# Optimization experiments

Hardware: AMD Instinct MI355X
Metric: run time of the kernel (lower is better)

Reference implementation:

```python
import jax, jax.numpy as jnp
import numpy as np

N, IN_DIM, HID, OUT_DIM, E, L = 100000, 128, 128, 64, 1600000, 4
ALPHA = 0.6


def gcn_conv(x, W, b, src, dst, deg_inv_sqrt):
    # PyG GCNConv: add self-loops, symmetric norm, linear, scatter-add, bias
    xw = x @ W                                    # [N, H]
    norm = deg_inv_sqrt[src] * deg_inv_sqrt[dst]  # [E]
    msg = xw[src] * norm[:, None]                 # [E, H] (memory-bound gather)
    agg = jax.ops.segment_sum(msg, dst, num_segments=N)
    # self-loop contribution: weight 1 * deg^-1
    agg = agg + xw * (deg_inv_sqrt * deg_inv_sqrt)[:, None]
    return agg + b


def setup_inputs() -> dict:
    key = jax.random.key(0)
    ks = jax.random.split(key, 8)
    s = 1.0 / np.sqrt(HID)
    x = jax.random.normal(ks[0], (N, IN_DIM), dtype=jnp.float32)
    edge_index = jax.random.randint(ks[1], (2, E), 0, N, dtype=jnp.int64)
    W1 = jax.random.uniform(ks[2], (IN_DIM, HID), jnp.float32, -s, s)
    b1 = jnp.zeros((HID,), jnp.float32)
    convW = jax.random.uniform(ks[3], (L, HID, HID), jnp.float32, -s, s)
    convB = jnp.zeros((L, HID), jnp.float32)
    W2 = jax.random.uniform(ks[4], (HID, OUT_DIM), jnp.float32, -s, s)
    b2 = jnp.zeros((OUT_DIM,), jnp.float32)
    return {"x": x, "edge_index": edge_index, "W1": W1, "b1": b1,
            "convW": convW, "convB": convB, "W2": W2, "b2": b2}


def reference(x, edge_index, W1, b1, convW, convB, W2, b2):
    src, dst = edge_index[0], edge_index[1]
    # degree with self-loops (gcn_norm with edge weight 1 on dst/col)
    deg = jax.ops.segment_sum(jnp.ones((E,), x.dtype), dst, num_segments=N) + 1.0
    deg_inv_sqrt = 1.0 / jnp.sqrt(deg)

    Z = x @ W1 + b1
    z_init = Z
    z_sum = jnp.zeros_like(Z)
    for i in range(L):
        Z = jax.nn.relu(gcn_conv(Z, convW[i], convB[i], src, dst, deg_inv_sqrt))
        z_sum = z_sum + Z
    out = ALPHA * z_init + (1.0 - ALPHA) * z_sum / L
    return out @ W2 + b2
```

## Files before the change

### kernel.cpp

```cpp
#include <hip/hip_runtime.h>

#define HID 128
#define NLAYERS 4
#define MAXBUCK 1600
#define CHUNK 16384

typedef __attribute__((ext_vector_type(8))) short bf16x8;
typedef __attribute__((ext_vector_type(8))) unsigned short u16x8;
typedef __attribute__((ext_vector_type(4))) float f32x4;

static __device__ __forceinline__ float bf2f(unsigned short u) {
    return __uint_as_float(((unsigned)u) << 16);
}
static __device__ __forceinline__ unsigned short f2bf(float f) {
    unsigned u = __float_as_uint(f);
    return (unsigned short)((u + 0x7FFF + ((u >> 16) & 1)) >> 16);
}


__global__ __launch_bounds__(256) void bin1(const int* __restrict__ dst,
                                            int* __restrict__ cnt2d, int E, int nbuck) {
    __shared__ int h[MAXBUCK];
    int tid = threadIdx.x;
    for (int i = tid; i < nbuck; i += 256) h[i] = 0;
    __syncthreads();
    int e0 = blockIdx.x * CHUNK;
    int e1 = min(e0 + CHUNK, E);
    for (int e = e0 + tid; e < e1; e += 256) atomicAdd(&h[dst[e] >> 6], 1);
    __syncthreads();
    for (int i = tid; i < nbuck; i += 256)
        cnt2d[(size_t)blockIdx.x * nbuck + i] = h[i];
}

__global__ void colscan(int* __restrict__ cnt2d, int* __restrict__ colsum,
                        int nchunks, int nbuck) {
    int b = blockIdx.x * blockDim.x + threadIdx.x;
    if (b >= nbuck) return;
    int run = 0;
    for (int c = 0; c < nchunks; ++c) {
        size_t idx = (size_t)c * nbuck + b;
        int v = cnt2d[idx];
        cnt2d[idx] = run;
        run += v;
    }
    colsum[b] = run;
}

__global__ __launch_bounds__(256) void basescan(const int* __restrict__ colsum,
                                                int* __restrict__ base, int nbuck) {
    __shared__ int part[256];
    int tid = threadIdx.x;
    const int per = 7;
    int loc[per];
    int run = 0;
    for (int i = 0; i < per; ++i) {
        int idx = tid * per + i;
        int v = (idx < nbuck) ? colsum[idx] : 0;
        run += v;
        loc[i] = run;
    }
    part[tid] = run;
    __syncthreads();
    for (int off = 1; off < 256; off <<= 1) {
        int t = (tid >= off) ? part[tid - off] : 0;
        __syncthreads();
        part[tid] += t;
        __syncthreads();
    }
    int prev = tid ? part[tid - 1] : 0;
    if (tid == 0) base[0] = 0;
    for (int i = 0; i < per; ++i) {
        int idx = tid * per + i;
        if (idx < nbuck) base[idx + 1] = prev + loc[i];
    }
}

__global__ __launch_bounds__(256) void bin2(const int* __restrict__ src, const int* __restrict__ dst,
                                            const int* __restrict__ cnt2d, const int* __restrict__ base,
                                            unsigned* __restrict__ ecoarse, int E, int nbuck) {
    __shared__ int cur[MAXBUCK];
    int tid = threadIdx.x;
    for (int i = tid; i < nbuck; i += 256)
        cur[i] = base[i] + cnt2d[(size_t)blockIdx.x * nbuck + i];
    __syncthreads();
    int e0 = blockIdx.x * CHUNK;
    int e1 = min(e0 + CHUNK, E);
    for (int e = e0 + tid; e < e1; e += 256) {
        int d = dst[e];
        int b = d >> 6;
        int pos = atomicAdd(&cur[b], 1);
        ecoarse[pos] = (unsigned)src[e] | ((unsigned)(d & 63) << 20);
    }
}

__global__ __launch_bounds__(64) void degdis(const unsigned* __restrict__ ecoarse,
                                             const int* __restrict__ base,
                                             float* __restrict__ dis, int N) {
    __shared__ int cnt[64];
    int b = blockIdx.x, t = threadIdx.x;
    cnt[t] = 0;
    __syncthreads();
    int s = base[b], e = base[b + 1];
    for (int i = s + t; i < e; i += 64) atomicAdd(&cnt[ecoarse[i] >> 20], 1);
    __syncthreads();
    int node = b * 64 + t;
    if (node < N) dis[node] = rsqrtf((float)cnt[t] + 1.0f);
}

__global__ __launch_bounds__(256) void finesort(const unsigned* __restrict__ ecoarse,
                                                const int* __restrict__ base,
                                                const float* __restrict__ dis,
                                                int2* __restrict__ csr, int* __restrict__ rowp,
                                                int N, int E) {
    __shared__ int h[64], off[64];
    int b = blockIdx.x, tid = threadIdx.x;
    if (tid < 64) h[tid] = 0;
    __syncthreads();
    int s = base[b], e = base[b + 1];
    for (int i = s + tid; i < e; i += 256) atomicAdd(&h[ecoarse[i] >> 20], 1);
    __syncthreads();
    if (tid == 0) {
        int run = 0;
        for (int i = 0; i < 64; ++i) { off[i] = run; run += h[i]; }
    }
    __syncthreads();
    int node = b * 64 + tid;
    if (tid < 64 && node < N) rowp[node] = s + off[tid];
    if (b == 0 && tid == 0) rowp[N] = E;
    if (tid < 64) h[tid] = off[tid];
    __syncthreads();
    for (int i = s + tid; i < e; i += 256) {
        unsigned v = ecoarse[i];
        int srcn = v & 0xFFFFF;
        int dl = v >> 20;
        int pos = atomicAdd(&h[dl], 1);
        int2 o;
        o.x = srcn;
        o.y = __float_as_int(dis[srcn] * dis[b * 64 + dl]);
        csr[s + pos] = o;
    }
}


__global__ void wprep(const float* __restrict__ W1, const float* __restrict__ convW,
                      const float* __restrict__ W2, unsigned short* __restrict__ W1t,
                      unsigned short* __restrict__ convWt, unsigned short* __restrict__ W2t) {
    int r = blockIdx.x;
    int k = threadIdx.x;
    const float* src;
    unsigned short* dst;
    int ncols, n;
    if (r < 128) { src = W1; dst = W1t; n = r; ncols = 128; }
    else if (r < 640) {
        int l = (r - 128) >> 7; n = (r - 128) & 127;
        src = convW + (size_t)l * 16384; dst = convWt + (size_t)l * 16384; ncols = 128;
    } else { src = W2; dst = W2t; n = r - 640; ncols = 64; }
    dst[(size_t)n * 128 + k] = f2bf(src[(size_t)k * ncols + n]);
}

__global__ void xcast(const float* __restrict__ x, unsigned short* __restrict__ xb, int n8) {
    int i = blockIdx.x * blockDim.x + threadIdx.x;
    if (i >= n8) return;
    float4 v0 = *(const float4*)&x[(size_t)i * 8];
    float4 v1 = *(const float4*)&x[(size_t)i * 8 + 4];
    u16x8 o;
    o[0] = f2bf(v0.x); o[1] = f2bf(v0.y); o[2] = f2bf(v0.z); o[3] = f2bf(v0.w);
    o[4] = f2bf(v1.x); o[5] = f2bf(v1.y); o[6] = f2bf(v1.z); o[7] = f2bf(v1.w);
    *(u16x8*)&xb[(size_t)i * 8] = o;
}


template <bool BIAS>
__global__ __launch_bounds__(256, 2) void gemm128_mfma(
    const unsigned short* __restrict__ A, const unsigned short* __restrict__ Bt,
    const float* __restrict__ bias, unsigned short* __restrict__ C, int nrows) {
    int wid = threadIdx.x >> 6, lane = threadIdx.x & 63;
    int l15 = lane & 15, l4 = lane >> 4;

    bf16x8 b[8][4];
#pragma unroll
    for (int nt = 0; nt < 8; ++nt)
#pragma unroll
        for (int ks = 0; ks < 4; ++ks)
            b[nt][ks] = *(const bf16x8*)&Bt[(size_t)(nt * 16 + l15) * 128 + ks * 32 + l4 * 8];
    float bb[8];
    if (BIAS) {
#pragma unroll
        for (int nt = 0; nt < 8; ++nt) bb[nt] = bias[nt * 16 + l15];
    }

    for (int s2 = 0; s2 < 2; ++s2) {
        int row0 = (blockIdx.x * 8 + wid * 2 + s2) * 16;
        if (row0 >= nrows) break;
        int ar = min(row0 + l15, nrows - 1);
        bf16x8 a[4];
#pragma unroll
        for (int ks = 0; ks < 4; ++ks)
            a[ks] = *(const bf16x8*)&A[(size_t)ar * 128 + ks * 32 + l4 * 8];
        f32x4 acc[8] = {};
#pragma unroll
        for (int ks = 0; ks < 4; ++ks)
#pragma unroll
            for (int nt = 0; nt < 8; ++nt)
                acc[nt] = __builtin_amdgcn_mfma_f32_16x16x32_bf16(a[ks], b[nt][ks], acc[nt], 0, 0, 0);
#pragma unroll
        for (int nt = 0; nt < 8; ++nt) {
            int col = nt * 16 + l15;
#pragma unroll
            for (int r = 0; r < 4; ++r) {
                int row = row0 + l4 * 4 + r;
                if (row < nrows) {
                    float v = acc[nt][r];
                    if (BIAS) v += bb[nt];
                    C[(size_t)row * 128 + col] = f2bf(v);
                }
            }
        }
    }
}


__global__ __launch_bounds__(256, 2) void gemm_final(
    const unsigned short* __restrict__ z0, const unsigned short* __restrict__ z1,
    const unsigned short* __restrict__ z2, const unsigned short* __restrict__ z3,
    const unsigned short* __restrict__ z4, const unsigned short* __restrict__ Bt,
    const float* __restrict__ bias, float* __restrict__ out, int nrows) {
    int wid = threadIdx.x >> 6, lane = threadIdx.x & 63;
    int l15 = lane & 15, l4 = lane >> 4;

    bf16x8 b[4][4];
#pragma unroll
    for (int nt = 0; nt < 4; ++nt)
#pragma unroll
        for (int ks = 0; ks < 4; ++ks)
            b[nt][ks] = *(const bf16x8*)&Bt[(size_t)(nt * 16 + l15) * 128 + ks * 32 + l4 * 8];
    float bb[4];
#pragma unroll
    for (int nt = 0; nt < 4; ++nt) bb[nt] = bias[nt * 16 + l15];

    const unsigned short* zs[5] = { z0, z1, z2, z3, z4 };

    for (int s2 = 0; s2 < 2; ++s2) {
        int row0 = (blockIdx.x * 8 + wid * 2 + s2) * 16;
        if (row0 >= nrows) break;
        int ar = min(row0 + l15, nrows - 1);
        bf16x8 a[5][4];
#pragma unroll
        for (int st = 0; st < 5; ++st)
#pragma unroll
            for (int ks = 0; ks < 4; ++ks)
                a[st][ks] = *(const bf16x8*)&zs[st][(size_t)ar * 128 + ks * 32 + l4 * 8];
        f32x4 acc0[4] = {};
        f32x4 acc1[4] = {};
#pragma unroll
        for (int st = 0; st < 5; ++st)
#pragma unroll
            for (int ks = 0; ks < 4; ++ks)
#pragma unroll
                for (int nt = 0; nt < 4; ++nt) {
                    if (st == 0)
                        acc0[nt] = __builtin_amdgcn_mfma_f32_16x16x32_bf16(a[0][ks], b[nt][ks], acc0[nt], 0, 0, 0);
                    else
                        acc1[nt] = __builtin_amdgcn_mfma_f32_16x16x32_bf16(a[st][ks], b[nt][ks], acc1[nt], 0, 0, 0);
                }
#pragma unroll
        for (int nt = 0; nt < 4; ++nt) {
            int col = nt * 16 + l15;
#pragma unroll
            for (int r = 0; r < 4; ++r) {
                int row = row0 + l4 * 4 + r;
                if (row < nrows)
                    out[(size_t)row * 64 + col] = 0.6f * acc0[nt][r] + 0.1f * acc1[nt][r] + bb[nt];
            }
        }
    }
}


__global__ __launch_bounds__(256) void spmm_kernel(
    const unsigned short* __restrict__ xwb, const int* __restrict__ rowp,
    const int2* __restrict__ csr, const float* __restrict__ dis,
    const float* __restrict__ bias, unsigned short* __restrict__ Z, int n) {
    int l = threadIdx.x & 15;
    int node = blockIdx.x * 16 + (threadIdx.x >> 4);
    if (node >= n) return;
    const u16x8* xw8 = (const u16x8*)xwb;

    float acc[8] = {};
    int beg = rowp[node], end = rowp[node + 1];
    int e = beg;
    for (; e + 4 <= end; e += 4) {
        int2 s0 = csr[e];
        int2 s1 = csr[e + 1];
        int2 s2 = csr[e + 2];
        int2 s3 = csr[e + 3];
        u16x8 x0 = xw8[(size_t)s0.x * 16 + l];
        u16x8 x1 = xw8[(size_t)s1.x * 16 + l];
        u16x8 x2 = xw8[(size_t)s2.x * 16 + l];
        u16x8 x3 = xw8[(size_t)s3.x * 16 + l];
        float w0 = __int_as_float(s0.y);
        float w1 = __int_as_float(s1.y);
        float w2 = __int_as_float(s2.y);
        float w3 = __int_as_float(s3.y);
#pragma unroll
        for (int j = 0; j < 8; ++j) {
            acc[j] = fmaf(w0, bf2f(x0[j]), acc[j]);
            acc[j] = fmaf(w1, bf2f(x1[j]), acc[j]);
            acc[j] = fmaf(w2, bf2f(x2[j]), acc[j]);
            acc[j] = fmaf(w3, bf2f(x3[j]), acc[j]);
        }
    }
    for (; e < end; ++e) {
        int2 s0 = csr[e];
        u16x8 x0 = xw8[(size_t)s0.x * 16 + l];
        float w0 = __int_as_float(s0.y);
#pragma unroll
        for (int j = 0; j < 8; ++j) acc[j] = fmaf(w0, bf2f(x0[j]), acc[j]);
    }

    float d = dis[node];
    float d2 = d * d;
    u16x8 xs = xw8[(size_t)node * 16 + l];
    float4 b0 = *(const float4*)&bias[l * 8];
    float4 b1 = *(const float4*)&bias[l * 8 + 4];
    float bbv[8] = { b0.x, b0.y, b0.z, b0.w, b1.x, b1.y, b1.z, b1.w };
    u16x8 ov;
#pragma unroll
    for (int j = 0; j < 8; ++j)
        ov[j] = f2bf(fmaxf(acc[j] + fmaf(d2, bf2f(xs[j]), bbv[j]), 0.f));
    *(u16x8*)&Z[(size_t)node * HID + l * 8] = ov;
}


extern "C" void kernel_launch(void* const* d_in, const int* in_sizes, int n_in,
                              void* d_out, int out_size, void* d_ws, size_t ws_size,
                              hipStream_t stream) {
    const float* x     = (const float*)d_in[0];
    const int*   ei    = (const int*)d_in[1];
    const float* W1    = (const float*)d_in[2];
    const float* b1    = (const float*)d_in[3];
    const float* convW = (const float*)d_in[4];
    const float* convB = (const float*)d_in[5];
    const float* W2    = (const float*)d_in[6];
    const float* b2    = (const float*)d_in[7];

    const int N = in_sizes[0] / HID;
    const int E = in_sizes[1] / 2;
    const int* src = ei;
    const int* dst = ei + E;
    const int nbuck = (N + 63) / 64;
    const int nchunks = (E + CHUNK - 1) / CHUNK;

    char* p = (char*)d_ws;
    auto alloc = [&](size_t bytes) {
        void* q = (void*)p;
        p += (bytes + 255) & ~(size_t)255;
        return q;
    };
    float* dis      = (float*)alloc((size_t)N * 4);
    int*   rowp     = (int*)alloc((size_t)(N + 1) * 4);
    int*   base     = (int*)alloc((size_t)(nbuck + 1) * 4);
    int*   colsum   = (int*)alloc((size_t)nbuck * 4);
    int*   cnt2d    = (int*)alloc((size_t)nchunks * nbuck * 4);
    unsigned* ecoarse = (unsigned*)alloc((size_t)E * 4);
    int2*  csr      = (int2*)alloc((size_t)E * 8);
    unsigned short* xb = (unsigned short*)alloc((size_t)N * HID * 2);
    unsigned short* xw = (unsigned short*)alloc((size_t)N * HID * 2);
    unsigned short* Zs[5];
    for (int i = 0; i < 4; ++i) Zs[i] = (unsigned short*)alloc((size_t)N * HID * 2);
    Zs[4] = xb;
    unsigned short* W1t    = (unsigned short*)alloc(128 * 128 * 2);
    unsigned short* convWt = (unsigned short*)alloc((size_t)NLAYERS * 128 * 128 * 2);
    unsigned short* W2t    = (unsigned short*)alloc(64 * 128 * 2);

    const int gemmBlocks = (N + 127) / 128;

    wprep<<<704, 128, 0, stream>>>(W1, convW, W2, W1t, convWt, W2t);
    xcast<<<(N * 16 + 255) / 256, 256, 0, stream>>>(x, xb, N * 16);

    bin1<<<nchunks, 256, 0, stream>>>(dst, cnt2d, E, nbuck);
    colscan<<<(nbuck + 255) / 256, 256, 0, stream>>>(cnt2d, colsum, nchunks, nbuck);
    basescan<<<1, 256, 0, stream>>>(colsum, base, nbuck);
    bin2<<<nchunks, 256, 0, stream>>>(src, dst, cnt2d, base, ecoarse, E, nbuck);
    degdis<<<nbuck, 64, 0, stream>>>(ecoarse, base, dis, N);
    finesort<<<nbuck, 256, 0, stream>>>(ecoarse, base, dis, csr, rowp, N, E);

    gemm128_mfma<true><<<gemmBlocks, 256, 0, stream>>>(xb, W1t, b1, Zs[0], N);

    for (int l = 0; l < NLAYERS; ++l) {
        gemm128_mfma<false><<<gemmBlocks, 256, 0, stream>>>(
            Zs[l], convWt + (size_t)l * 16384, nullptr, xw, N);
        spmm_kernel<<<(N + 15) / 16, 256, 0, stream>>>(
            xw, rowp, csr, dis, convB + (size_t)l * HID, Zs[l + 1], N);
    }

    gemm_final<<<gemmBlocks, 256, 0, stream>>>(
        Zs[0], Zs[1], Zs[2], Zs[3], Zs[4], W2t, b2, (float*)d_out, N);
}
```

Measured before the change: 666.7 us.

## Fold degree computation into finesort and shrink CSR to source indices only

Removes the separate degdis kernel by computing deg^-1/2 inside finesort from its per-node histogram. CSR entries shrink from int2 (src, weight) to a single unsigned src index. SpMM now gathers dis[src] per edge and applies the destination factor once at the end, which halves index traffic per layer at the cost of an extra small random gather. CHUNK drops to 2048 to give the binning kernels more blocks, which also enlarges the cnt2d array and the column scans.

```diff
diff --git a/kernel.cpp b/kernel.cpp
--- a/kernel.cpp
+++ b/kernel.cpp
@@ -3,7 +3,7 @@
 #define HID 128
 #define NLAYERS 4
 #define MAXBUCK 1600
-#define CHUNK 16384
+#define CHUNK 2048
 
 typedef __attribute__((ext_vector_type(8))) short bf16x8;
 typedef __attribute__((ext_vector_type(8))) unsigned short u16x8;
@@ -93,24 +93,10 @@
     }
 }
 
-__global__ __launch_bounds__(64) void degdis(const unsigned* __restrict__ ecoarse,
-                                             const int* __restrict__ base,
-                                             float* __restrict__ dis, int N) {
-    __shared__ int cnt[64];
-    int b = blockIdx.x, t = threadIdx.x;
-    cnt[t] = 0;
-    __syncthreads();
-    int s = base[b], e = base[b + 1];
-    for (int i = s + t; i < e; i += 64) atomicAdd(&cnt[ecoarse[i] >> 20], 1);
-    __syncthreads();
-    int node = b * 64 + t;
-    if (node < N) dis[node] = rsqrtf((float)cnt[t] + 1.0f);
-}
-
 __global__ __launch_bounds__(256) void finesort(const unsigned* __restrict__ ecoarse,
                                                 const int* __restrict__ base,
-                                                const float* __restrict__ dis,
-                                                int2* __restrict__ csr, int* __restrict__ rowp,
+                                                float* __restrict__ dis,
+                                                unsigned* __restrict__ csr, int* __restrict__ rowp,
                                                 int N, int E) {
     __shared__ int h[64], off[64];
     int b = blockIdx.x, tid = threadIdx.x;
@@ -124,20 +110,21 @@
         for (int i = 0; i < 64; ++i) { off[i] = run; run += h[i]; }
     }
     __syncthreads();
-    int node = b * 64 + tid;
-    if (tid < 64 && node < N) rowp[node] = s + off[tid];
+    if (tid < 64) {
+        int node = b * 64 + tid;
+        if (node < N) {
+            rowp[node] = s + off[tid];
+            dis[node] = rsqrtf((float)h[tid] + 1.0f);
+        }
+        h[tid] = off[tid];
+    }
     if (b == 0 && tid == 0) rowp[N] = E;
-    if (tid < 64) h[tid] = off[tid];
     __syncthreads();
     for (int i = s + tid; i < e; i += 256) {
         unsigned v = ecoarse[i];
-        int srcn = v & 0xFFFFF;
         int dl = v >> 20;
         int pos = atomicAdd(&h[dl], 1);
-        int2 o;
-        o.x = srcn;
-        o.y = __float_as_int(dis[srcn] * dis[b * 64 + dl]);
-        csr[s + pos] = o;
+        csr[s + pos] = v & 0xFFFFF;
     }
 }
 
@@ -279,7 +266,7 @@
 
 __global__ __launch_bounds__(256) void spmm_kernel(
     const unsigned short* __restrict__ xwb, const int* __restrict__ rowp,
-    const int2* __restrict__ csr, const float* __restrict__ dis,
+    const unsigned* __restrict__ csr, const float* __restrict__ dis,
     const float* __restrict__ bias, unsigned short* __restrict__ Z, int n) {
     int l = threadIdx.x & 15;
     int node = blockIdx.x * 16 + (threadIdx.x >> 4);
@@ -290,18 +277,18 @@
     int beg = rowp[node], end = rowp[node + 1];
     int e = beg;
     for (; e + 4 <= end; e += 4) {
-        int2 s0 = csr[e];
-        int2 s1 = csr[e + 1];
-        int2 s2 = csr[e + 2];
-        int2 s3 = csr[e + 3];
-        u16x8 x0 = xw8[(size_t)s0.x * 16 + l];
-        u16x8 x1 = xw8[(size_t)s1.x * 16 + l];
-        u16x8 x2 = xw8[(size_t)s2.x * 16 + l];
-        u16x8 x3 = xw8[(size_t)s3.x * 16 + l];
-        float w0 = __int_as_float(s0.y);
-        float w1 = __int_as_float(s1.y);
-        float w2 = __int_as_float(s2.y);
-        float w3 = __int_as_float(s3.y);
+        unsigned s0 = csr[e];
+        unsigned s1 = csr[e + 1];
+        unsigned s2 = csr[e + 2];
+        unsigned s3 = csr[e + 3];
+        float w0 = dis[s0];
+        float w1 = dis[s1];
+        float w2 = dis[s2];
+        float w3 = dis[s3];
+        u16x8 x0 = xw8[(size_t)s0 * 16 + l];
+        u16x8 x1 = xw8[(size_t)s1 * 16 + l];
+        u16x8 x2 = xw8[(size_t)s2 * 16 + l];
+        u16x8 x3 = xw8[(size_t)s3 * 16 + l];
 #pragma unroll
         for (int j = 0; j < 8; ++j) {
             acc[j] = fmaf(w0, bf2f(x0[j]), acc[j]);
@@ -311,9 +298,9 @@
         }
     }
     for (; e < end; ++e) {
-        int2 s0 = csr[e];
-        u16x8 x0 = xw8[(size_t)s0.x * 16 + l];
-        float w0 = __int_as_float(s0.y);
+        unsigned s0 = csr[e];
+        float w0 = dis[s0];
+        u16x8 x0 = xw8[(size_t)s0 * 16 + l];
 #pragma unroll
         for (int j = 0; j < 8; ++j) acc[j] = fmaf(w0, bf2f(x0[j]), acc[j]);
     }
@@ -327,7 +314,7 @@
     u16x8 ov;
 #pragma unroll
     for (int j = 0; j < 8; ++j)
-        ov[j] = f2bf(fmaxf(acc[j] + fmaf(d2, bf2f(xs[j]), bbv[j]), 0.f));
+        ov[j] = f2bf(fmaxf(fmaf(d, acc[j], fmaf(d2, bf2f(xs[j]), bbv[j])), 0.f));
     *(u16x8*)&Z[(size_t)node * HID + l * 8] = ov;
 }
 
@@ -363,7 +350,7 @@
     int*   colsum   = (int*)alloc((size_t)nbuck * 4);
     int*   cnt2d    = (int*)alloc((size_t)nchunks * nbuck * 4);
     unsigned* ecoarse = (unsigned*)alloc((size_t)E * 4);
-    int2*  csr      = (int2*)alloc((size_t)E * 8);
+    unsigned* csr   = (unsigned*)alloc((size_t)E * 4);
     unsigned short* xb = (unsigned short*)alloc((size_t)N * HID * 2);
     unsigned short* xw = (unsigned short*)alloc((size_t)N * HID * 2);
     unsigned short* Zs[5];
@@ -382,7 +369,6 @@
     colscan<<<(nbuck + 255) / 256, 256, 0, stream>>>(cnt2d, colsum, nchunks, nbuck);
     basescan<<<1, 256, 0, stream>>>(colsum, base, nbuck);
     bin2<<<nchunks, 256, 0, stream>>>(src, dst, cnt2d, base, ecoarse, E, nbuck);
-    degdis<<<nbuck, 64, 0, stream>>>(ecoarse, base, dis, N);
     finesort<<<nbuck, 256, 0, stream>>>(ecoarse, base, dis, csr, rowp, N, E);
 
     gemm128_mfma<true><<<gemmBlocks, 256, 0, stream>>>(xb, W1t, b1, Zs[0], N);
```

Result: slower. 761.7 us (+14.2%).
